# Performance work log

Hardware: AMD Instinct MI355X
Metric: run time of the kernel (lower is better)

Reference implementation:

```python
import jax, jax.numpy as jnp
import numpy as np

INPUTSIZE = 1024
OUTPUTSIZE = 1024
FEATUREMAPS = 16
BITS = (INPUTSIZE - 1).bit_length()  # 10
BATCH = 2048


def _make_fm():
    # fm[k, j, i] = (i ^ (1 << j)) % inputsize  (same for every feature map k)
    i = np.arange(OUTPUTSIZE, dtype=np.int64)
    j = (1 << np.arange(BITS, dtype=np.int64))[:, None]
    fm_bits_out = (i[None, :] ^ j) % INPUTSIZE  # [bits, out]
    fm = np.broadcast_to(fm_bits_out[None], (FEATUREMAPS, BITS, OUTPUTSIZE)).copy()
    return jnp.asarray(fm, dtype=jnp.int32)


def setup_inputs() -> dict:
    key = jax.random.key(0)
    k1, k2, k3 = jax.random.split(key, 3)
    std = 0.5 / BITS
    x = jax.random.normal(k1, (BATCH, INPUTSIZE), dtype=jnp.float32)
    weights = jax.random.normal(k2, (FEATUREMAPS, BITS, OUTPUTSIZE), dtype=jnp.float32) * std
    bias = jax.random.normal(k3, (FEATUREMAPS, OUTPUTSIZE), dtype=jnp.float32) * std
    return {"x": x, "weights": weights, "bias": bias, "fm": _make_fm()}


def _resize(t, newsize):
    # Static-shape version of Layer.resize (column crop/tile)
    cur = t.shape[1]
    if newsize < cur:
        return t[:, :newsize]
    if newsize > cur:
        mult = (newsize + cur - 1) // cur
        return jnp.tile(t, (1, mult))[:, :newsize]
    return t


def reference(x, weights, bias, fm):
    # gather: [B, F, bits, O]
    gathered = x[:, fm]
    # multiply by weights [F, bits, O] and reduce over bits -> [B, F, O]
    net = jnp.einsum('bfjo,fjo->bfo', gathered, weights) + bias
    flat = net.reshape(x.shape[0], FEATUREMAPS * OUTPUTSIZE)
    tiled = jnp.tile(_resize(x, OUTPUTSIZE), (1, FEATUREMAPS))
    return flat + tiled
```

## Files before the change

### kernel.cpp

```cpp
#include <hip/hip_runtime.h>


#define BTILE 16
#define NSLOT 5

__global__ __launch_bounds__(128, 2) void hypercube_kernel(
    const float* __restrict__ x,
    const float* __restrict__ w,
    const float* __restrict__ bias,
    float* __restrict__ out)
{
    __shared__ float xs[BTILE * NSLOT * 64];

    const int tid   = threadIdx.x;
    const int lane  = tid & 63;
    const int wave  = tid >> 6;
    const int chunk = blockIdx.x & 15;
    const int btile = blockIdx.x >> 4;
    const int b0    = btile * BTILE;
    const int f0    = wave * 8;
    const int o     = chunk * 64 + lane;

    #pragma unroll
    for (int it = 0; it < (BTILE * NSLOT * 64 / 4) / 128; ++it) {
        const int q    = it * 128 + tid;
        const int row  = q / (NSLOT * 16);
        const int rem  = q - row * (NSLOT * 16);
        const int slot = rem >> 4;
        const int l4   = (rem & 15) << 2;
        const int src_chunk = chunk ^ ((1 << slot) >> 1);
        const float4 v = *(const float4*)&x[(size_t)(b0 + row) * 1024 + src_chunk * 64 + l4];
        *(float4*)&xs[q * 4] = v;
    }

    float wr[8][10], br[8];
    #pragma unroll
    for (int ff = 0; ff < 8; ++ff) {
        const int f = f0 + ff;
        #pragma unroll
        for (int j = 0; j < 10; ++j)
            wr[ff][j] = w[(f * 10 + j) * 1024 + o];
        br[ff] = bias[f * 1024 + o];
    }

    __syncthreads();

    #pragma unroll 2
    for (int row = 0; row < BTILE; ++row) {
        const float* __restrict__ xr = &xs[row * (NSLOT * 64)];
        const float x0 = xr[lane];
        const float g0 = xr[lane ^ 1];
        const float g1 = xr[lane ^ 2];
        const float g2 = xr[lane ^ 4];
        const float g3 = xr[lane ^ 8];
        const float g4 = xr[lane ^ 16];
        const float g5 = xr[lane ^ 32];
        const float g6 = xr[64  + lane];
        const float g7 = xr[128 + lane];
        const float g8 = xr[192 + lane];
        const float g9 = xr[256 + lane];

        float* __restrict__ ob = out + (size_t)(b0 + row) * 16384 + chunk * 64 + lane;
        #pragma unroll
        for (int ff = 0; ff < 8; ++ff) {
            float acc = br[ff] + x0;
            acc = fmaf(g0, wr[ff][0], acc);
            acc = fmaf(g1, wr[ff][1], acc);
            acc = fmaf(g2, wr[ff][2], acc);
            acc = fmaf(g3, wr[ff][3], acc);
            acc = fmaf(g4, wr[ff][4], acc);
            acc = fmaf(g5, wr[ff][5], acc);
            acc = fmaf(g6, wr[ff][6], acc);
            acc = fmaf(g7, wr[ff][7], acc);
            acc = fmaf(g8, wr[ff][8], acc);
            acc = fmaf(g9, wr[ff][9], acc);
            ob[(f0 + ff) * 1024] = acc;
        }
    }
}

extern "C" void kernel_launch(void* const* d_in, const int* in_sizes, int n_in,
                              void* d_out, int out_size, void* d_ws, size_t ws_size,
                              hipStream_t stream) {
    const float* x    = (const float*)d_in[0];
    const float* w    = (const float*)d_in[1];
    const float* bias = (const float*)d_in[2];
    float* out = (float*)d_out;

    dim3 grid(16 * (2048 / BTILE));
    dim3 block(128);
    hypercube_kernel<<<grid, block, 0, stream>>>(x, w, bias, out);
}
```

Measured before the change: 149.9 us.

## Vectorize hypercube kernel to float4 per lane with wider output tiles

Each lane now handles four consecutive outputs using float4 loads of x, weights and bias, and float4 stores. The low two XOR bits are resolved inside the float4 by shuffling components, which cuts shared-memory traffic. The block layout changes to 256 threads covering a 256-wide output quarter and half the feature maps, with 3 float4 slots per row. This reduces the number of load and store instructions on a store-bound kernel, at the cost of higher register pressure and changed occupancy.

```diff
diff --git a/kernel.cpp b/kernel.cpp
--- a/kernel.cpp
+++ b/kernel.cpp
@@ -2,79 +2,79 @@
 
 
 #define BTILE 16
-#define NSLOT 5
 
-__global__ __launch_bounds__(128, 2) void hypercube_kernel(
+__global__ __launch_bounds__(256, 3) void hypercube_kernel(
     const float* __restrict__ x,
     const float* __restrict__ w,
     const float* __restrict__ bias,
     float* __restrict__ out)
 {
-    __shared__ float xs[BTILE * NSLOT * 64];
+    __shared__ float4 xs4[BTILE * 3 * 64];
 
     const int tid   = threadIdx.x;
     const int lane  = tid & 63;
     const int wave  = tid >> 6;
-    const int chunk = blockIdx.x & 15;
-    const int btile = blockIdx.x >> 4;
+    const int q     = blockIdx.x & 3;
+    const int fh    = (blockIdx.x >> 2) & 1;
+    const int btile = blockIdx.x >> 3;
     const int b0    = btile * BTILE;
-    const int f0    = wave * 8;
-    const int o     = chunk * 64 + lane;
+    const int f0    = fh * 8 + wave * 2;
+    const int obase = q * 256 + lane * 4;
 
     #pragma unroll
-    for (int it = 0; it < (BTILE * NSLOT * 64 / 4) / 128; ++it) {
-        const int q    = it * 128 + tid;
-        const int row  = q / (NSLOT * 16);
-        const int rem  = q - row * (NSLOT * 16);
-        const int slot = rem >> 4;
-        const int l4   = (rem & 15) << 2;
-        const int src_chunk = chunk ^ ((1 << slot) >> 1);
-        const float4 v = *(const float4*)&x[(size_t)(b0 + row) * 1024 + src_chunk * 64 + l4];
-        *(float4*)&xs[q * 4] = v;
+    for (int it = 0; it < 12; ++it) {
+        const int i    = it * 256 + tid;
+        const int row  = i / 192;
+        const int rem  = i - row * 192;
+        const int slot = rem >> 6;
+        const int l4   = rem & 63;
+        xs4[i] = *(const float4*)&x[(size_t)(b0 + row) * 1024 + (q ^ slot) * 256 + l4 * 4];
     }
 
-    float wr[8][10], br[8];
+    float4 wr[2][10], br[2];
     #pragma unroll
-    for (int ff = 0; ff < 8; ++ff) {
+    for (int ff = 0; ff < 2; ++ff) {
         const int f = f0 + ff;
         #pragma unroll
         for (int j = 0; j < 10; ++j)
-            wr[ff][j] = w[(f * 10 + j) * 1024 + o];
-        br[ff] = bias[f * 1024 + o];
+            wr[ff][j] = *(const float4*)&w[(size_t)(f * 10 + j) * 1024 + obase];
+        br[ff] = *(const float4*)&bias[(size_t)f * 1024 + obase];
     }
 
     __syncthreads();
 
-    #pragma unroll 2
+    #pragma unroll 1
     for (int row = 0; row < BTILE; ++row) {
-        const float* __restrict__ xr = &xs[row * (NSLOT * 64)];
-        const float x0 = xr[lane];
-        const float g0 = xr[lane ^ 1];
-        const float g1 = xr[lane ^ 2];
-        const float g2 = xr[lane ^ 4];
-        const float g3 = xr[lane ^ 8];
-        const float g4 = xr[lane ^ 16];
-        const float g5 = xr[lane ^ 32];
-        const float g6 = xr[64  + lane];
-        const float g7 = xr[128 + lane];
-        const float g8 = xr[192 + lane];
-        const float g9 = xr[256 + lane];
+        const float4* __restrict__ xr = &xs4[row * 192];
+        const float4 v  = xr[lane];
+        const float4 g2 = xr[lane ^ 1];
+        const float4 g3 = xr[lane ^ 2];
+        const float4 g4 = xr[lane ^ 4];
+        const float4 g5 = xr[lane ^ 8];
+        const float4 g6 = xr[lane ^ 16];
+        const float4 g7 = xr[lane ^ 32];
+        const float4 g8 = xr[64  + lane];
+        const float4 g9 = xr[128 + lane];
+        const float4 g0 = make_float4(v.y, v.x, v.w, v.z);
+        const float4 g1 = make_float4(v.z, v.w, v.x, v.y);
 
-        float* __restrict__ ob = out + (size_t)(b0 + row) * 16384 + chunk * 64 + lane;
+        float* __restrict__ ob = out + (size_t)(b0 + row) * 16384 + obase;
         #pragma unroll
-        for (int ff = 0; ff < 8; ++ff) {
-            float acc = br[ff] + x0;
-            acc = fmaf(g0, wr[ff][0], acc);
-            acc = fmaf(g1, wr[ff][1], acc);
-            acc = fmaf(g2, wr[ff][2], acc);
-            acc = fmaf(g3, wr[ff][3], acc);
-            acc = fmaf(g4, wr[ff][4], acc);
-            acc = fmaf(g5, wr[ff][5], acc);
-            acc = fmaf(g6, wr[ff][6], acc);
-            acc = fmaf(g7, wr[ff][7], acc);
-            acc = fmaf(g8, wr[ff][8], acc);
-            acc = fmaf(g9, wr[ff][9], acc);
-            ob[(f0 + ff) * 1024] = acc;
+        for (int ff = 0; ff < 2; ++ff) {
+            float4 a;
+            a.x = br[ff].x + v.x;
+            a.y = br[ff].y + v.y;
+            a.z = br[ff].z + v.z;
+            a.w = br[ff].w + v.w;
+            #define FMA4(G, J) \
+                a.x = fmaf((G).x, wr[ff][J].x, a.x); \
+                a.y = fmaf((G).y, wr[ff][J].y, a.y); \
+                a.z = fmaf((G).z, wr[ff][J].z, a.z); \
+                a.w = fmaf((G).w, wr[ff][J].w, a.w);
+            FMA4(g0, 0) FMA4(g1, 1) FMA4(g2, 2) FMA4(g3, 3) FMA4(g4, 4)
+            FMA4(g5, 5) FMA4(g6, 6) FMA4(g7, 7) FMA4(g8, 8) FMA4(g9, 9)
+            #undef FMA4
+            *(float4*)&ob[(size_t)(f0 + ff) * 1024] = a;
         }
     }
 }
@@ -87,7 +87,7 @@
     const float* bias = (const float*)d_in[2];
     float* out = (float*)d_out;
 
-    dim3 grid(16 * (2048 / BTILE));
-    dim3 block(128);
+    dim3 grid(4 * 2 * (2048 / BTILE));
+    dim3 block(256);
     hypercube_kernel<<<grid, block, 0, stream>>>(x, w, bias, out);
 }
```

Result: slower. 381.3 us (+154.4%).
